# Performance work log

Measured on AMD Instinct MI355X. Metric: run time of the kernel, lower is better.

Reference implementation:

```python
import jax, jax.numpy as jnp
import numpy as np

TAU = 2.0      # spikingjelly LIFNode tau
V_TH = 1.0     # default v_threshold
ALPHA = 2.0    # default ATan surrogate alpha
T_STEPS = 32   # output_size (repeat count along time)

# Heaviside spike with ATan surrogate gradient (spikingjelly surrogate.ATan)
@jax.custom_vjp
def spike_fn(x):
    return (x >= 0.0).astype(x.dtype)

def _spike_fwd(x):
    return spike_fn(x), x

def _spike_bwd(x, g):
    sg = (ALPHA / 2.0) / (1.0 + (jnp.pi / 2.0 * ALPHA * x) ** 2)
    return (g * sg,)

spike_fn.defvjp(_spike_fwd, _spike_bwd)


def setup_inputs() -> dict:
    key = jax.random.key(0)
    inputs = jax.random.normal(key, (64, 64, 512), dtype=jnp.float32)  # [B, C, L]
    return {"inputs": inputs}


def reference(inputs):
    # repeat([T,1,1,1]) then permute(0,1,3,2): every step sees the same [B,L,C] frame
    xt = jnp.transpose(inputs, (0, 2, 1))  # [B, L, C]
    v0 = jnp.zeros_like(xt)                # v_reset = 0.0 initial membrane

    def step(v, _):
        # LIF with decay_input=True, hard reset to v_reset=0:
        # v = v + (x - (v - v_reset)) / tau
        v = v + (xt - v) / TAU
        s = spike_fn(v - V_TH)
        # hard reset; detach_reset=True -> spike detached in reset path
        v = v * (1.0 - jax.lax.stop_gradient(s))
        return v, s

    _, spks = jax.lax.scan(step, v0, None, length=T_STEPS)  # [T, B, L, C]
    return jnp.transpose(spks, (1, 0, 2, 3))                # [B, T, L, C]
```

## Files before the change

kernel.cpp:

```cpp
#include <hip/hip_runtime.h>


constexpr int B = 64;
constexpr int C = 64;
constexpr int L = 512;
constexpr int T = 32;

typedef float vf4 __attribute__((ext_vector_type(4)));

__global__ __launch_bounds__(256) void lif_repeat_kernel(
    const float* __restrict__ in, float* __restrict__ out) {
  __shared__ float lds[64 * 64];
  const int tid = threadIdx.x;
  const int b  = blockIdx.x >> 3;
  const int l0 = (blockIdx.x & 7) * 64;

  {
    const int c = tid >> 2;
    const int q = tid & 3;
    const float* ip = in + (size_t)b * (C * L) + (size_t)c * L + l0;
#pragma unroll
    for (int k = 0; k < 4; ++k) {
      const int lo = q * 4 + k * 16;
      const vf4 v = *(const vf4*)(ip + lo);
      lds[(lo + 0) * 64 + c] = v.x;
      lds[(lo + 1) * 64 + c] = v.y;
      lds[(lo + 2) * 64 + c] = v.z;
      lds[(lo + 3) * 64 + c] = v.w;
    }
  }
  __syncthreads();

  const int c4 = tid & 15;
  const int rr = tid >> 4;
  float x[4][4], v[4][4];
#pragma unroll
  for (int j = 0; j < 4; ++j) {
    const vf4 xv = *(const vf4*)(lds + (rr + 16 * j) * 64 + c4 * 4);
    x[j][0] = xv.x; x[j][1] = xv.y; x[j][2] = xv.z; x[j][3] = xv.w;
    v[j][0] = v[j][1] = v[j][2] = v[j][3] = 0.f;
  }

  float* const obase = out + (size_t)b * (T * L * C) + (size_t)l0 * C + c4 * 4;
  constexpr size_t t_stride = (size_t)L * C;

#pragma unroll 2
  for (int t = 0; t < T; ++t) {
    float* ot = obase + (size_t)t * t_stride;
#pragma unroll
    for (int j = 0; j < 4; ++j) {
      vf4 s;
#pragma unroll
      for (int i = 0; i < 4; ++i) {
        v[j][i] += (x[j][i] - v[j][i]) * 0.5f;
      }
      s.x = (v[j][0] >= 1.0f) ? 1.0f : 0.0f;
      s.y = (v[j][1] >= 1.0f) ? 1.0f : 0.0f;
      s.z = (v[j][2] >= 1.0f) ? 1.0f : 0.0f;
      s.w = (v[j][3] >= 1.0f) ? 1.0f : 0.0f;
      *(vf4*)(ot + (size_t)(rr + 16 * j) * C) = s;
#pragma unroll
      for (int i = 0; i < 4; ++i) {
        v[j][i] = (v[j][i] >= 1.0f) ? 0.0f : v[j][i];
      }
    }
  }
}

extern "C" void kernel_launch(void* const* d_in, const int* in_sizes, int n_in,
                              void* d_out, int out_size, void* d_ws, size_t ws_size,
                              hipStream_t stream) {
  const float* in = (const float*)d_in[0];
  float* out = (float*)d_out;
  const int grid = B * (L / 64);
  lif_repeat_kernel<<<grid, 256, 0, stream>>>(in, out);
}
```

Baseline: 268.1 us.

## Split time steps across blocks with recompute prefix, larger tiles, swizzled LDS

Reworks the decomposition so that each block handles half of L (256 positions), all channels, and a quarter of the 32 time steps, using 512 threads. Each block recomputes the membrane recurrence for the earlier time steps without storing anything, then writes its own 8 steps. The LDS transpose gains an XOR swizzle to avoid bank conflicts. The grid stays at 512 blocks, but each block's output is now more concentrated, and the input is read four times. The exchange is redundant prefix compute and register pressure from 64 floats of state per thread.

```diff
diff --git a/kernel.cpp b/kernel.cpp
--- a/kernel.cpp
+++ b/kernel.cpp
@@ -5,50 +5,70 @@
 constexpr int C = 64;
 constexpr int L = 512;
 constexpr int T = 32;
+constexpr int LC = L * C;
+constexpr int LH = 256;
+constexpr int TQ = 8;
 
 typedef float vf4 __attribute__((ext_vector_type(4)));
 
-__global__ __launch_bounds__(256) void lif_repeat_kernel(
+__global__ __launch_bounds__(512) void lif_repeat_kernel(
     const float* __restrict__ in, float* __restrict__ out) {
-  __shared__ float lds[64 * 64];
+  __shared__ float lds[LH * C];
   const int tid = threadIdx.x;
-  const int b  = blockIdx.x >> 3;
-  const int l0 = (blockIdx.x & 7) * 64;
+  const int bid = blockIdx.x;
+  const int q  = bid & 3;
+  const int lh = (bid >> 2) & 1;
+  const int b  = bid >> 3;
+  const int t0 = q * TQ;
 
   {
-    const int c = tid >> 2;
-    const int q = tid & 3;
-    const float* ip = in + (size_t)b * (C * L) + (size_t)c * L + l0;
+    const int crow = tid >> 3;
+    const int q8   = tid & 7;
+    const int cl = crow & 3;
+    const int ch = crow >> 2;
+    const float* ip = in + (size_t)b * (C * L) + (size_t)crow * L + lh * LH;
 #pragma unroll
-    for (int k = 0; k < 4; ++k) {
-      const int lo = q * 4 + k * 16;
-      const vf4 v = *(const vf4*)(ip + lo);
-      lds[(lo + 0) * 64 + c] = v.x;
-      lds[(lo + 1) * 64 + c] = v.y;
-      lds[(lo + 2) * 64 + c] = v.z;
-      lds[(lo + 3) * 64 + c] = v.w;
+    for (int k = 0; k < 8; ++k) {
+      const int lo = q8 * 4 + k * 32;
+      const vf4 xv = *(const vf4*)(ip + lo);
+      const int sw = cl + 4 * ((ch ^ (q8 + 8 * (k & 1))) & 15);
+#pragma unroll
+      for (int i = 0; i < 4; ++i) {
+        lds[(lo + i) * 64 + sw] = xv[i];
+      }
     }
   }
   __syncthreads();
 
   const int c4 = tid & 15;
   const int rr = tid >> 4;
-  float x[4][4], v[4][4];
+  float x[8][4], v[8][4];
 #pragma unroll
-  for (int j = 0; j < 4; ++j) {
-    const vf4 xv = *(const vf4*)(lds + (rr + 16 * j) * 64 + c4 * 4);
+  for (int j = 0; j < 8; ++j) {
+    const int ll = rr + 32 * j;
+    const int g = c4 ^ ((ll >> 2) & 15);
+    const vf4 xv = *(const vf4*)(lds + ll * 64 + 4 * g);
     x[j][0] = xv.x; x[j][1] = xv.y; x[j][2] = xv.z; x[j][3] = xv.w;
     v[j][0] = v[j][1] = v[j][2] = v[j][3] = 0.f;
   }
 
-  float* const obase = out + (size_t)b * (T * L * C) + (size_t)l0 * C + c4 * 4;
-  constexpr size_t t_stride = (size_t)L * C;
+  for (int t = 0; t < t0; ++t) {
+#pragma unroll
+    for (int j = 0; j < 8; ++j) {
+#pragma unroll
+      for (int i = 0; i < 4; ++i) {
+        const float vv = v[j][i] + (x[j][i] - v[j][i]) * 0.5f;
+        v[j][i] = (vv >= 1.0f) ? 0.0f : vv;
+      }
+    }
+  }
 
+  float* op = out + (size_t)b * (T * LC) + (size_t)t0 * LC
+                  + (size_t)(lh * LH + rr) * C + c4 * 4;
 #pragma unroll 2
-  for (int t = 0; t < T; ++t) {
-    float* ot = obase + (size_t)t * t_stride;
+  for (int tt = 0; tt < TQ; ++tt) {
 #pragma unroll
-    for (int j = 0; j < 4; ++j) {
+    for (int j = 0; j < 8; ++j) {
       vf4 s;
 #pragma unroll
       for (int i = 0; i < 4; ++i) {
@@ -58,12 +78,13 @@
       s.y = (v[j][1] >= 1.0f) ? 1.0f : 0.0f;
       s.z = (v[j][2] >= 1.0f) ? 1.0f : 0.0f;
       s.w = (v[j][3] >= 1.0f) ? 1.0f : 0.0f;
-      *(vf4*)(ot + (size_t)(rr + 16 * j) * C) = s;
+      *(vf4*)(op + (size_t)(32 * j) * C) = s;
 #pragma unroll
       for (int i = 0; i < 4; ++i) {
         v[j][i] = (v[j][i] >= 1.0f) ? 0.0f : v[j][i];
       }
     }
+    op += LC;
   }
 }
 
@@ -72,6 +93,6 @@
                               hipStream_t stream) {
   const float* in = (const float*)d_in[0];
   float* out = (float*)d_out;
-  const int grid = B * (L / 64);
-  lif_repeat_kernel<<<grid, 256, 0, stream>>>(in, out);
+  const int grid = B * 2 * 4;
+  lif_repeat_kernel<<<grid, 512, 0, stream>>>(in, out);
 }
```

After: 278.9 us. 1.04x slower.
